# Performance work log

Measured on AMD Instinct MI355X. Metric: run time of the kernel, lower is better.

The kernel has to match this reference:

```python
import jax, jax.numpy as jnp
import numpy as np

U = 128  # LSTM units (hardcoded in module)


def _lstm(x_tm, W, Urec, b, return_sequences):
    """Keras-style LSTM. x_tm: [T,B,F] time-major. Gate order i,f,c(g),o.
    activation=tanh, recurrent_activation=sigmoid. recurrent_dropout is
    inference-mode identity (dropout only active in training)."""
    T, B, _ = x_tm.shape
    xz = jnp.einsum('tbf,fg->tbg', x_tm, W) + b  # precompute input projections [T,B,4U]

    def step(carry, xz_t):
        h, c = carry
        z = xz_t + h @ Urec  # [B,4U]
        i, f, g, o = jnp.split(z, 4, axis=-1)
        i = jax.nn.sigmoid(i)
        f = jax.nn.sigmoid(f)
        g = jnp.tanh(g)
        o = jax.nn.sigmoid(o)
        c_new = f * c + i * g
        h_new = o * jnp.tanh(c_new)
        return (h_new, c_new), h_new

    h0 = jnp.zeros((B, U), x_tm.dtype)
    c0 = jnp.zeros((B, U), x_tm.dtype)
    (h_last, _), hs = jax.lax.scan(step, (h0, c0), xz)
    return hs if return_sequences else h_last


def setup_inputs() -> dict:
    key = jax.random.key(0)
    ks = jax.random.split(key, 7)
    B, T, F = 512, 256, 64
    s_in = 1.0 / np.sqrt(F)
    s_rec = 1.0 / np.sqrt(U)
    return {
        'x': jax.random.normal(ks[0], (B, T, F), jnp.float32),
        'W1': jax.random.normal(ks[1], (F, 4 * U), jnp.float32) * s_in,
        'U1': jax.random.normal(ks[2], (U, 4 * U), jnp.float32) * s_rec,
        'b1': jnp.zeros((4 * U,), jnp.float32),
        'W2': jax.random.normal(ks[3], (U, 4 * U), jnp.float32) * s_rec,
        'U2': jax.random.normal(ks[4], (U, 4 * U), jnp.float32) * s_rec,
        'b2': jnp.zeros((4 * U,), jnp.float32),
        'Wd': jax.random.normal(ks[5], (U, 1), jnp.float32) * s_rec,
        'bd': jnp.zeros((1,), jnp.float32),
    }


def reference(x, W1, U1, b1, W2, U2, b2, Wd, bd):
    x_tm = jnp.transpose(x, (1, 0, 2))  # [T,B,F]
    hs = _lstm(x_tm, W1, U1, b1, return_sequences=True)   # hidden_lstm -> [T,B,U]
    h_last = _lstm(hs, W2, U2, b2, return_sequences=False)  # lstm_layer -> [B,U]
    return jax.nn.relu(h_last @ Wd + bd)  # Dense(1, relu) -> [B,1]
```

## Files before the change

kernel.cpp:

```cpp
#include <hip/hip_runtime.h>


#define T_STEPS 256
#define BATCH   512
#define NU      128
#define FDIM    64

typedef _Float16 h8 __attribute__((ext_vector_type(8)));
typedef _Float16 h4 __attribute__((ext_vector_type(4)));
typedef float    f4 __attribute__((ext_vector_type(4)));

#define LOG2E    1.4426950408889634f
#define TWOLOG2E 2.8853900817779268f

#if __has_builtin(__builtin_amdgcn_exp2f)
#define EXP2F(x) __builtin_amdgcn_exp2f(x)
#else
#define EXP2F(x) exp2f(x)
#endif
#if __has_builtin(__builtin_amdgcn_rcpf)
#define RCPF(x) __builtin_amdgcn_rcpf(x)
#else
#define RCPF(x) (1.0f / (x))
#endif

__device__ __forceinline__ float sigm2(float s) {
    return RCPF(1.0f + EXP2F(-s));
}
__device__ __forceinline__ float tanh2(float t) {
    return 1.0f - 2.0f * RCPF(1.0f + EXP2F(t));
}

__global__ void prep_weights(const float* __restrict__ W1, const float* __restrict__ U1,
                             const float* __restrict__ b1, const float* __restrict__ W2,
                             const float* __restrict__ U2, const float* __restrict__ b2,
                             _Float16* __restrict__ Wp1, _Float16* __restrict__ Up1,
                             _Float16* __restrict__ Wp2, _Float16* __restrict__ Up2,
                             float* __restrict__ bp1, float* __restrict__ bp2) {
    int i = blockIdx.x * 256 + threadIdx.x;
    if (i < 32768) {
        int col = i >> 6, k = i & 63;
        float sc = ((col >> 7) == 2) ? TWOLOG2E : LOG2E;
        Wp1[i] = (_Float16)(W1[k * 512 + col] * sc);
    } else if (i < 32768 + 65536) {
        int j = i - 32768; int col = j >> 7, k = j & 127;
        float sc = ((col >> 7) == 2) ? TWOLOG2E : LOG2E;
        Up1[j] = (_Float16)(U1[k * 512 + col] * sc);
    } else if (i < 32768 + 131072) {
        int j = i - 98304; int col = j >> 7, k = j & 127;
        float sc = ((col >> 7) == 2) ? TWOLOG2E : LOG2E;
        Wp2[j] = (_Float16)(W2[k * 512 + col] * sc);
    } else if (i < 32768 + 196608) {
        int j = i - 163840; int col = j >> 7, k = j & 127;
        float sc = ((col >> 7) == 2) ? TWOLOG2E : LOG2E;
        Up2[j] = (_Float16)(U2[k * 512 + col] * sc);
    } else if (i < 32768 + 196608 + 1024) {
        int j = i - 229376;
        if (j < 512) {
            float sc = ((j >> 7) == 2) ? TWOLOG2E : LOG2E;
            bp1[j] = b1[j] * sc;
        } else {
            int col = j - 512;
            float sc = ((col >> 7) == 2) ? TWOLOG2E : LOG2E;
            bp2[col] = b2[col] * sc;
        }
    }
}

template <bool IS_A>
__attribute__((amdgpu_waves_per_eu(2, 2)))
__global__ __launch_bounds__(512) void lstm_layer(
    const float* __restrict__ xA, const _Float16* __restrict__ xB,
    const _Float16* __restrict__ Wp,
    const _Float16* __restrict__ Up,
    const float* __restrict__ bp,
    _Float16* __restrict__ hs_out,
    const float* __restrict__ Wd, const float* __restrict__ bd,
    float* __restrict__ dout) {
    constexpr int KX  = IS_A ? 64 : 128;
    constexpr int KXS = KX / 32;
    constexpr int PH  = 136;
    constexpr int H0  = 0;
    constexpr int H1  = 2 * PH;
    constexpr int XZ  = 4 * PH;
    constexpr int XZH = 8 * NU * 8;
    constexpr int SMH = XZ + 2 * XZH;

    __shared__ __align__(16) _Float16 sm[SMH];

    const int tid  = threadIdx.x;
    const int lane = tid & 63;
    const int wv   = tid >> 6;
    const int m    = lane & 15;
    const int kc   = lane >> 4;
    const int u0   = wv * 16;
    const int b0   = blockIdx.x * 2;

    for (int i = tid; i < 4 * PH; i += 512) sm[i] = (_Float16)0.0f;

    h8 uf[4][4];
#pragma unroll
    for (int g = 0; g < 4; g++)
#pragma unroll
        for (int ks = 0; ks < 4; ks++)
            uf[g][ks] = *(const h8*)&Up[(g * 128 + u0 + m) * 128 + ks * 32 + kc * 8];
    h8 wf[4][KXS];
#pragma unroll
    for (int g = 0; g < 4; g++)
#pragma unroll
        for (int ks = 0; ks < KXS; ks++)
            wf[g][ks] = *(const h8*)&Wp[(g * 128 + u0 + m) * KX + ks * 32 + kc * 8];
    float bias[4];
#pragma unroll
    for (int g = 0; g < 4; g++) bias[g] = bp[g * 128 + u0 + m];

    f4 rX[4]; h8 rH[4];
    auto loadA = [&](int kblk) {
        int tt = kblk * 8 + (m >> 1); if (tt > T_STEPS - 1) tt = T_STEPS - 1;
        const int bb = b0 + (m & 1);
        if constexpr (IS_A) {
#pragma unroll
            for (int ks = 0; ks < KXS; ks++)
#pragma unroll
                for (int hf = 0; hf < 2; hf++)
                    rX[ks * 2 + hf] = *(const f4*)&xA[((size_t)bb * T_STEPS + tt) * FDIM
                                                      + ks * 32 + kc * 8 + hf * 4];
        } else {
#pragma unroll
            for (int ks = 0; ks < 4; ks++)
                rH[ks] = *(const h8*)&xB[((size_t)tt * BATCH + bb) * NU + ks * 32 + kc * 8];
        }
    };
    auto calcX = [&](int kblk) {
        _Float16* xzw = &sm[XZ + (kblk & 1) * XZH];
        f4 accx[4];
#pragma unroll
        for (int g = 0; g < 4; g++) accx[g] = (f4){bias[g], bias[g], bias[g], bias[g]};
#pragma unroll
        for (int ks = 0; ks < KXS; ks++) {
            h8 a;
            if constexpr (IS_A) {
#pragma unroll
                for (int j = 0; j < 4; j++) {
                    a[j]     = (_Float16)rX[ks * 2][j];
                    a[4 + j] = (_Float16)rX[ks * 2 + 1][j];
                }
            } else {
                a = rH[ks];
            }
#pragma unroll
            for (int g = 0; g < 4; g++)
                accx[g] = __builtin_amdgcn_mfma_f32_16x16x32_f16(a, wf[g][ks], accx[g], 0, 0, 0);
        }
#pragma unroll
        for (int g = 0; g < 4; g++)
#pragma unroll
            for (int r = 0; r < 4; r++) {
                int r16 = kc * 4 + r;
                xzw[(((r16 >> 1) * 128 + u0 + m) * 2 + (r16 & 1)) * 4 + g] =
                    (_Float16)accx[g][r];
            }
    };

    loadA(0); calcX(0);
    loadA(1);
    __syncthreads();

    const h8 hzero = {};
    h8 ha[4];
#pragma unroll
    for (int ks = 0; ks < 4; ks++) ha[ks] = hzero;

    float c0 = 0.0f, c1 = 0.0f;

#pragma unroll 8
    for (int t = 0; t < T_STEPS; t++) {
        const int p = t & 1;
        const int s = t & 7;

        if (s == 0) {
            int kn = (t >> 3) + 1;
            if (kn < T_STEPS / 8) {
                calcX(kn);
                loadA(kn + 1);
            }
        }

        h8 xzf = hzero;
        if (lane < 16)
            xzf = *(const h8*)&sm[XZ + ((t >> 3) & 1) * XZH + (s * 128 + u0 + m) * 8];
        f4 acc[4];
#pragma unroll
        for (int g = 0; g < 4; g++)
            acc[g] = (f4){(float)xzf[g], (float)xzf[4 + g], 0.0f, 0.0f};

        if (m < 2) {
            const _Float16* hb = &sm[p ? H1 : H0];
#pragma unroll
            for (int ks = 0; ks < 4; ks++)
                ha[ks] = *(const h8*)&hb[m * PH + ks * 32 + kc * 8];
        }
#pragma unroll
        for (int ks = 0; ks < 4; ks++)
#pragma unroll
            for (int g = 0; g < 4; g++)
                acc[g] = __builtin_amdgcn_mfma_f32_16x16x32_f16(ha[ks], uf[g][ks], acc[g], 0, 0, 0);

        if (lane < 16) {
            float gi0 = sigm2(acc[0][0]), gf0 = sigm2(acc[1][0]);
            float gg0 = tanh2(acc[2][0]), go0 = sigm2(acc[3][0]);
            c0 = gf0 * c0 + gi0 * gg0;
            float hv0 = go0 * tanh2(c0 * TWOLOG2E);
            float gi1 = sigm2(acc[0][1]), gf1 = sigm2(acc[1][1]);
            float gg1 = tanh2(acc[2][1]), go1 = sigm2(acc[3][1]);
            c1 = gf1 * c1 + gi1 * gg1;
            float hv1 = go1 * tanh2(c1 * TWOLOG2E);
            _Float16 h0v = (_Float16)hv0, h1v = (_Float16)hv1;
            _Float16* hbn = &sm[p ? H0 : H1];
            hbn[u0 + m] = h0v;
            hbn[PH + u0 + m] = h1v;
            if constexpr (IS_A) {
                hs_out[((size_t)t * BATCH + b0    ) * NU + u0 + m] = h0v;
                hs_out[((size_t)t * BATCH + b0 + 1) * NU + u0 + m] = h1v;
            }
        }
        __syncthreads();
    }

    if constexpr (!IS_A) {
        if (wv == 0) {
            int rw = lane >> 5, u = lane & 31;
            float sacc = 0.0f;
#pragma unroll
            for (int j = 0; j < 4; j++) {
                int uum = u + j * 32;
                sacc += (float)sm[H0 + rw * PH + uum] * Wd[uum];
            }
            sacc += __shfl_xor(sacc, 16);
            sacc += __shfl_xor(sacc, 8);
            sacc += __shfl_xor(sacc, 4);
            sacc += __shfl_xor(sacc, 2);
            sacc += __shfl_xor(sacc, 1);
            if ((lane & 31) == 0) dout[b0 + rw] = fmaxf(sacc + bd[0], 0.0f);
        }
    }
}

extern "C" void kernel_launch(void* const* d_in, const int* in_sizes, int n_in,
                              void* d_out, int out_size, void* d_ws, size_t ws_size,
                              hipStream_t stream) {
    const float* x  = (const float*)d_in[0];
    const float* W1 = (const float*)d_in[1];
    const float* U1 = (const float*)d_in[2];
    const float* b1 = (const float*)d_in[3];
    const float* W2 = (const float*)d_in[4];
    const float* U2 = (const float*)d_in[5];
    const float* b2 = (const float*)d_in[6];
    const float* Wd = (const float*)d_in[7];
    const float* bd = (const float*)d_in[8];
    float* out = (float*)d_out;

    const size_t HS   = 33554432;
    const size_t oWp1 = HS;
    const size_t oUp1 = oWp1 + 65536;
    const size_t oWp2 = oUp1 + 131072;
    const size_t oUp2 = oWp2 + 131072;
    const size_t oBp1 = oUp2 + 131072;
    const size_t oBp2 = oBp1 + 2048;
    const size_t need = oBp2 + 2048;
    if (ws_size < need) return;

    char* ws = (char*)d_ws;
    _Float16* hs  = (_Float16*)ws;
    _Float16* Wp1 = (_Float16*)(ws + oWp1);
    _Float16* Up1 = (_Float16*)(ws + oUp1);
    _Float16* Wp2 = (_Float16*)(ws + oWp2);
    _Float16* Up2 = (_Float16*)(ws + oUp2);
    float*    bp1 = (float*)(ws + oBp1);
    float*    bp2 = (float*)(ws + oBp2);

    prep_weights<<<900, 256, 0, stream>>>(W1, U1, b1, W2, U2, b2,
                                          Wp1, Up1, Wp2, Up2, bp1, bp2);
    lstm_layer<true><<<256, 512, 0, stream>>>(x, nullptr, Wp1, Up1, bp1,
                                              hs, nullptr, nullptr, nullptr);
    lstm_layer<false><<<256, 512, 0, stream>>>(nullptr, hs, Wp2, Up2, bp2,
                                               nullptr, Wd, bd, out);
}
```

Before: 418.0 us.

## Spread LSTM gate math across 32 lanes and keep input projections in fp32 LDS

The batch rows of h are placed into MFMA rows 0 and 4, so each 16-lane group gets one batch element, and the per-step gate math runs on 32 lanes each handling one row instead of 16 lanes handling two. The precomputed input projections are now stored as fp32 in LDS and added after the recurrent MFMA rather than used as the accumulator init. The sigmoid negation is folded into the packed weights. __syncthreads is replaced by a raw lgkmcnt wait plus s_barrier. The aim is to shorten the serial per-step critical path, at the cost of doubling the LDS used for the input projections.

```diff
diff --git a/kernel.cpp b/kernel.cpp
--- a/kernel.cpp
+++ b/kernel.cpp
@@ -12,6 +12,8 @@
 
 #define LOG2E    1.4426950408889634f
 #define TWOLOG2E 2.8853900817779268f
+
+#define WG_BARRIER() asm volatile("s_waitcnt lgkmcnt(0)\n\ts_barrier" ::: "memory")
 
 #if __has_builtin(__builtin_amdgcn_exp2f)
 #define EXP2F(x) __builtin_amdgcn_exp2f(x)
@@ -25,7 +27,7 @@
 #endif
 
 __device__ __forceinline__ float sigm2(float s) {
-    return RCPF(1.0f + EXP2F(-s));
+    return RCPF(1.0f + EXP2F(s));
 }
 __device__ __forceinline__ float tanh2(float t) {
     return 1.0f - 2.0f * RCPF(1.0f + EXP2F(t));
@@ -40,28 +42,28 @@
     int i = blockIdx.x * 256 + threadIdx.x;
     if (i < 32768) {
         int col = i >> 6, k = i & 63;
-        float sc = ((col >> 7) == 2) ? TWOLOG2E : LOG2E;
+        float sc = ((col >> 7) == 2) ? TWOLOG2E : -LOG2E;
         Wp1[i] = (_Float16)(W1[k * 512 + col] * sc);
     } else if (i < 32768 + 65536) {
         int j = i - 32768; int col = j >> 7, k = j & 127;
-        float sc = ((col >> 7) == 2) ? TWOLOG2E : LOG2E;
+        float sc = ((col >> 7) == 2) ? TWOLOG2E : -LOG2E;
         Up1[j] = (_Float16)(U1[k * 512 + col] * sc);
     } else if (i < 32768 + 131072) {
         int j = i - 98304; int col = j >> 7, k = j & 127;
-        float sc = ((col >> 7) == 2) ? TWOLOG2E : LOG2E;
+        float sc = ((col >> 7) == 2) ? TWOLOG2E : -LOG2E;
         Wp2[j] = (_Float16)(W2[k * 512 + col] * sc);
     } else if (i < 32768 + 196608) {
         int j = i - 163840; int col = j >> 7, k = j & 127;
-        float sc = ((col >> 7) == 2) ? TWOLOG2E : LOG2E;
+        float sc = ((col >> 7) == 2) ? TWOLOG2E : -LOG2E;
         Up2[j] = (_Float16)(U2[k * 512 + col] * sc);
     } else if (i < 32768 + 196608 + 1024) {
         int j = i - 229376;
         if (j < 512) {
-            float sc = ((j >> 7) == 2) ? TWOLOG2E : LOG2E;
+            float sc = ((j >> 7) == 2) ? TWOLOG2E : -LOG2E;
             bp1[j] = b1[j] * sc;
         } else {
             int col = j - 512;
-            float sc = ((col >> 7) == 2) ? TWOLOG2E : LOG2E;
+            float sc = ((col >> 7) == 2) ? TWOLOG2E : -LOG2E;
             bp2[col] = b2[col] * sc;
         }
     }
@@ -82,11 +84,9 @@
     constexpr int PH  = 136;
     constexpr int H0  = 0;
     constexpr int H1  = 2 * PH;
-    constexpr int XZ  = 4 * PH;
-    constexpr int XZH = 8 * NU * 8;
-    constexpr int SMH = XZ + 2 * XZH;
-
-    __shared__ __align__(16) _Float16 sm[SMH];
+
+    __shared__ __align__(16) _Float16 smh[4 * PH];
+    __shared__ __align__(16) float smxz[2 * 8 * 128 * 2 * 4];
 
     const int tid  = threadIdx.x;
     const int lane = tid & 63;
@@ -96,7 +96,7 @@
     const int u0   = wv * 16;
     const int b0   = blockIdx.x * 2;
 
-    for (int i = tid; i < 4 * PH; i += 512) sm[i] = (_Float16)0.0f;
+    for (int i = tid; i < 4 * PH; i += 512) smh[i] = (_Float16)0.0f;
 
     h8 uf[4][4];
 #pragma unroll
@@ -132,7 +132,7 @@
         }
     };
     auto calcX = [&](int kblk) {
-        _Float16* xzw = &sm[XZ + (kblk & 1) * XZH];
+        float* xzw = &smxz[(kblk & 1) * 8192];
         f4 accx[4];
 #pragma unroll
         for (int g = 0; g < 4; g++) accx[g] = (f4){bias[g], bias[g], bias[g], bias[g]};
@@ -155,10 +155,9 @@
 #pragma unroll
         for (int g = 0; g < 4; g++)
 #pragma unroll
-            for (int r = 0; r < 4; r++) {
-                int r16 = kc * 4 + r;
-                xzw[(((r16 >> 1) * 128 + u0 + m) * 2 + (r16 & 1)) * 4 + g] =
-                    (_Float16)accx[g][r];
+            for (int rr = 0; rr < 4; rr++) {
+                int r16 = kc * 4 + rr;
+                xzw[(((r16 >> 1) * 128 + u0 + m) * 2 + (r16 & 1)) * 4 + g] = accx[g][rr];
             }
     };
 
@@ -171,7 +170,8 @@
 #pragma unroll
     for (int ks = 0; ks < 4; ks++) ha[ks] = hzero;
 
-    float c0 = 0.0f, c1 = 0.0f;
+    const int erow = lane >> 4;
+    float cst = 0.0f;
 
 #pragma unroll 8
     for (int t = 0; t < T_STEPS; t++) {
@@ -186,45 +186,37 @@
             }
         }
 
-        h8 xzf = hzero;
-        if (lane < 16)
-            xzf = *(const h8*)&sm[XZ + ((t >> 3) & 1) * XZH + (s * 128 + u0 + m) * 8];
+        if (m == 0 || m == 4) {
+            const _Float16* hb = &smh[(p ? H1 : H0) + (m == 4 ? PH : 0)];
+#pragma unroll
+            for (int ks = 0; ks < 4; ks++)
+                ha[ks] = *(const h8*)&hb[ks * 32 + kc * 8];
+        }
+
         f4 acc[4];
 #pragma unroll
-        for (int g = 0; g < 4; g++)
-            acc[g] = (f4){(float)xzf[g], (float)xzf[4 + g], 0.0f, 0.0f};
-
-        if (m < 2) {
-            const _Float16* hb = &sm[p ? H1 : H0];
-#pragma unroll
-            for (int ks = 0; ks < 4; ks++)
-                ha[ks] = *(const h8*)&hb[m * PH + ks * 32 + kc * 8];
-        }
+        for (int g = 0; g < 4; g++) acc[g] = (f4){0.f, 0.f, 0.f, 0.f};
 #pragma unroll
         for (int ks = 0; ks < 4; ks++)
 #pragma unroll
             for (int g = 0; g < 4; g++)
                 acc[g] = __builtin_amdgcn_mfma_f32_16x16x32_f16(ha[ks], uf[g][ks], acc[g], 0, 0, 0);
 
-        if (lane < 16) {
-            float gi0 = sigm2(acc[0][0]), gf0 = sigm2(acc[1][0]);
-            float gg0 = tanh2(acc[2][0]), go0 = sigm2(acc[3][0]);
-            c0 = gf0 * c0 + gi0 * gg0;
-            float hv0 = go0 * tanh2(c0 * TWOLOG2E);
-            float gi1 = sigm2(acc[0][1]), gf1 = sigm2(acc[1][1]);
-            float gg1 = tanh2(acc[2][1]), go1 = sigm2(acc[3][1]);
-            c1 = gf1 * c1 + gi1 * gg1;
-            float hv1 = go1 * tanh2(c1 * TWOLOG2E);
-            _Float16 h0v = (_Float16)hv0, h1v = (_Float16)hv1;
-            _Float16* hbn = &sm[p ? H0 : H1];
-            hbn[u0 + m] = h0v;
-            hbn[PH + u0 + m] = h1v;
-            if constexpr (IS_A) {
-                hs_out[((size_t)t * BATCH + b0    ) * NU + u0 + m] = h0v;
-                hs_out[((size_t)t * BATCH + b0 + 1) * NU + u0 + m] = h1v;
-            }
-        }
-        __syncthreads();
+        if (lane < 32) {
+            const f4 xzv = *(const f4*)&smxz[((t >> 3) & 1) * 8192
+                                             + ((s * 128 + u0 + m) * 2 + erow) * 4];
+            float gi = sigm2(acc[0][0] + xzv[0]);
+            float gf = sigm2(acc[1][0] + xzv[1]);
+            float gg = tanh2(acc[2][0] + xzv[2]);
+            float go = sigm2(acc[3][0] + xzv[3]);
+            cst = gf * cst + gi * gg;
+            float hv = go * tanh2(cst * TWOLOG2E);
+            _Float16 h16 = (_Float16)hv;
+            smh[(p ? H0 : H1) + erow * PH + u0 + m] = h16;
+            if constexpr (IS_A)
+                hs_out[((size_t)t * BATCH + b0 + erow) * NU + u0 + m] = h16;
+        }
+        WG_BARRIER();
     }
 
     if constexpr (!IS_A) {
@@ -234,7 +226,7 @@
 #pragma unroll
             for (int j = 0; j < 4; j++) {
                 int uum = u + j * 32;
-                sacc += (float)sm[H0 + rw * PH + uum] * Wd[uum];
+                sacc += (float)smh[H0 + rw * PH + uum] * Wd[uum];
             }
             sacc += __shfl_xor(sacc, 16);
             sacc += __shfl_xor(sacc, 8);
```

New measurement: 358.2 us. 14.3% less time.
